# Kernel optimization log

Hardware: AMD Instinct MI355X
Metric: run time of the kernel (lower is better)

## Reference

```python
import jax, jax.numpy as jnp
import numpy as np

NUM_GROUPS = 32
EPS = 1e-5


def group_norm(x, w, b):
    # x: [B, C, H, W]
    B, C, H, W = x.shape
    xg = x.reshape(B, NUM_GROUPS, C // NUM_GROUPS, H, W)
    mean = jnp.mean(xg, axis=(2, 3, 4), keepdims=True)
    var = jnp.var(xg, axis=(2, 3, 4), keepdims=True)
    xg = (xg - mean) * jax.lax.rsqrt(var + EPS)
    xn = xg.reshape(B, C, H, W)
    return xn * w[None, :, None, None] + b[None, :, None, None]


def conv1x1(x, w, b):
    # x: [B, C, H, W], w: [O, C], b: [O]
    return jnp.einsum('bchw,oc->bohw', x, w) + b[None, :, None, None]


def setup_inputs() -> dict:
    key = jax.random.key(0)
    ks = jax.random.split(key, 10)
    C = 512
    x = jax.random.normal(ks[0], (4, C, 64, 64), dtype=jnp.float32)
    s = 1.0 / np.sqrt(C)
    return {
        'x': x,
        'gn_w': jnp.ones((C,), jnp.float32),
        'gn_b': jnp.zeros((C,), jnp.float32),
        'q_w': jax.random.normal(ks[1], (C, C), jnp.float32) * s,
        'q_b': jax.random.normal(ks[2], (C,), jnp.float32) * 0.01,
        'k_w': jax.random.normal(ks[3], (C, C), jnp.float32) * s,
        'k_b': jax.random.normal(ks[4], (C,), jnp.float32) * 0.01,
        'v_w': jax.random.normal(ks[5], (C, C), jnp.float32) * s,
        'v_b': jax.random.normal(ks[6], (C,), jnp.float32) * 0.01,
        'p_w': jax.random.normal(ks[7], (C, C), jnp.float32) * s,
        'p_b': jax.random.normal(ks[8], (C,), jnp.float32) * 0.01,
    }


def reference(x, gn_w, gn_b, q_w, q_b, k_w, k_b, v_w, v_b, p_w, p_b):
    h_ = group_norm(x, gn_w, gn_b)
    q = conv1x1(h_, q_w, q_b)
    k = conv1x1(h_, k_w, k_b)
    v = conv1x1(h_, v_w, v_b)
    b, c, h, w = q.shape
    n = h * w
    q = q.reshape(b, c, n).transpose(0, 2, 1)   # [b, n, c]
    k = k.reshape(b, c, n)                       # [b, c, n]
    scores = jnp.einsum('bic,bcj->bij', q, k) * (c ** -0.5)  # [b, n, n]
    attn = jax.nn.softmax(scores, axis=-1)
    v = v.reshape(b, c, n)                       # [b, c, n]
    # h_[b,c,i] = sum_j v[b,c,j] * attn[b,i,j]
    h_out = jnp.einsum('bcj,bij->bci', v, attn).reshape(b, c, h, w)
    return x + conv1x1(h_out, p_w, p_b)
```

## Files before the change

kernel.cpp:

```cpp
#include <hip/hip_runtime.h>
#include <hip/hip_bf16.h>
#include <stdint.h>

#define AS1 __attribute__((address_space(1)))
#define AS3 __attribute__((address_space(3)))

typedef unsigned short ushort_t;
typedef __attribute__((ext_vector_type(8))) short short8;
typedef __attribute__((ext_vector_type(4))) float floatx4;
typedef __attribute__((ext_vector_type(16))) float floatx16;
typedef __attribute__((ext_vector_type(2))) unsigned int uint2v;

__device__ __forceinline__ ushort_t f2b(float f) {
    union { float f; unsigned int i; } x; x.f = f;
    unsigned int r = x.i + 0x7fffu + ((x.i >> 16) & 1u);
    return (ushort_t)(r >> 16);
}
__device__ __forceinline__ float b2f(ushort_t u) {
    union { unsigned int i; float f; } x; x.i = ((unsigned int)u) << 16; return x.f;
}
__device__ __forceinline__ void gl2lds16(const void* g, void* l) {
    __builtin_amdgcn_global_load_lds(
        (const AS1 unsigned int*)g,
        (AS3 unsigned int*)l,
        16, 0, 0);
}
__device__ __forceinline__ void plswap(unsigned& a, unsigned& b) {
#if __has_builtin(__builtin_amdgcn_permlane32_swap)
    uint2v r = __builtin_amdgcn_permlane32_swap(a, b, false, false);
    a = r.x; b = r.y;
#else
    asm volatile("v_permlane32_swap_b32 %0, %1" : "+v"(a), "+v"(b));
#endif
}

static constexpr int CCH = 512;
static constexpr int NSP = 4096;
static constexpr int NG  = 32;

__global__ __launch_bounds__(256) void gn_stats(const float* __restrict__ x,
                                                float* __restrict__ mean,
                                                float* __restrict__ rstd) {
    const long base = (long)blockIdx.x * 65536;
    const int t = threadIdx.x;
    float s1 = 0.f, s2 = 0.f;
    for (int i = t * 8; i < 65536; i += 256 * 8) {
        float4 a = *(const float4*)(x + base + i);
        float4 b = *(const float4*)(x + base + i + 4);
        s1 += a.x + a.y + a.z + a.w + b.x + b.y + b.z + b.w;
        s2 += a.x * a.x + a.y * a.y + a.z * a.z + a.w * a.w
            + b.x * b.x + b.y * b.y + b.z * b.z + b.w * b.w;
    }
#pragma unroll
    for (int o = 32; o; o >>= 1) { s1 += __shfl_xor(s1, o, 64); s2 += __shfl_xor(s2, o, 64); }
    __shared__ float r1[4], r2[4];
    const int lane = t & 63, wave = t >> 6;
    if (!lane) { r1[wave] = s1; r2[wave] = s2; }
    __syncthreads();
    if (!t) {
        float S1 = r1[0] + r1[1] + r1[2] + r1[3];
        float S2 = r2[0] + r2[1] + r2[2] + r2[3];
        float mu = S1 * (1.f / 65536.f);
        float var = S2 * (1.f / 65536.f) - mu * mu;
        mean[blockIdx.x] = mu;
        rstd[blockIdx.x] = rsqrtf(var + 1e-5f);
    }
}

__global__ __launch_bounds__(256) void w_to_bf16(const float* __restrict__ q,
                                                 const float* __restrict__ k,
                                                 const float* __restrict__ v,
                                                 const float* __restrict__ p,
                                                 const float* __restrict__ qb,
                                                 ushort_t* __restrict__ out,
                                                 float* __restrict__ sqb) {
    const float scl = 0.044194173824159216f;
    const float* srcs[4] = { q, k, v, p };
    const float* s = srcs[blockIdx.y];
    const float m = (blockIdx.y == 0) ? scl : 1.f;
    const long i = ((long)blockIdx.x * 256 + threadIdx.x) * 4;
    float4 f = *(const float4*)(s + i);
    ushort_t o[4] __attribute__((aligned(8)));
    o[0] = f2b(f.x * m); o[1] = f2b(f.y * m); o[2] = f2b(f.z * m); o[3] = f2b(f.w * m);
    *(ushort4*)(out + (long)blockIdx.y * 262144 + i) = *(ushort4*)o;
    if (blockIdx.y == 0 && blockIdx.x == 0 && threadIdx.x < 128) {
        const int j = threadIdx.x * 4;
        float4 b = *(const float4*)(qb + j);
        sqb[j] = b.x * scl; sqb[j + 1] = b.y * scl; sqb[j + 2] = b.z * scl; sqb[j + 3] = b.w * scl;
    }
}

__global__ __launch_bounds__(256) void norm_transpose(const float* __restrict__ x,
                                                      const float* __restrict__ gw,
                                                      const float* __restrict__ gb,
                                                      const float* __restrict__ mean,
                                                      const float* __restrict__ rstd,
                                                      ushort_t* __restrict__ ht) {
    __shared__ ushort_t tile[64 * 65];
    const int b = blockIdx.z, c0 = blockIdx.y * 64, n0 = blockIdx.x * 64;
    const int t = threadIdx.x;
    const float* xb = x + ((long)b * CCH + c0) * NSP + n0;
#pragma unroll
    for (int p = 0; p < 2; ++p) {
        int li = p * 2048 + t * 8;
        int cl = li >> 6, nl = li & 63;
        int c = c0 + cl, g = c >> 4;
        float mu = mean[b * NG + g], rs = rstd[b * NG + g];
        float w  = gw[c] * rs;
        float bb = gb[c] - mu * w;
        float4 a = *(const float4*)(xb + (long)cl * NSP + nl);
        float4 d = *(const float4*)(xb + (long)cl * NSP + nl + 4);
        float f[8] = { a.x, a.y, a.z, a.w, d.x, d.y, d.z, d.w };
#pragma unroll
        for (int j = 0; j < 8; ++j) tile[cl * 65 + nl + j] = f2b(f[j] * w + bb);
    }
    __syncthreads();
#pragma unroll
    for (int p = 0; p < 2; ++p) {
        int li = p * 2048 + t * 8;
        int nl = li >> 6, cl = li & 63;
        ushort_t v[8] __attribute__((aligned(16)));
#pragma unroll
        for (int j = 0; j < 8; ++j) v[j] = tile[(cl + j) * 65 + nl];
        *(uint4*)(ht + ((long)b * NSP + n0 + nl) * CCH + c0 + cl) = *(uint4*)v;
    }
}

template <int BIAS, int OUTF32, int RES>
__global__ __launch_bounds__(256, 2) void gemm_tn(
    const ushort_t* __restrict__ A, int lda, long sA,
    const ushort_t* __restrict__ B, int ldb, long sB,
    void* __restrict__ Cp, int ldc, long sC,
    const float* __restrict__ bias,
    const float* __restrict__ resid, long sR,
    float scale, int K) {
    __shared__ short As[128 * 32];
    __shared__ short Bs[128 * 32];
    const int t = threadIdx.x;
    const int lane = t & 63, wave = t >> 6;
    const long bz = blockIdx.z;
    const int m0 = blockIdx.y * 128, n0 = blockIdx.x * 128;

    const ushort_t* Ab = A + bz * sA + (long)(m0 + (t >> 2)) * lda + (t & 3) * 8;
    const ushort_t* Bb = B + bz * sB + (long)(n0 + (t >> 2)) * ldb + (t & 3) * 8;
    short* la = As + t * 8;
    short* lb = Bs + t * 8;

    const int wm = (wave & 1) * 64, wn = (wave >> 1) * 64;
    const int lm = lane & 15, lk = (lane >> 4) * 8;
    const short* pa = As + (wm + lm) * 32 + lk;
    const short* pb = Bs + (wn + lm) * 32 + lk;

    floatx4 acc[4][4];
#pragma unroll
    for (int i = 0; i < 4; ++i)
#pragma unroll
        for (int j = 0; j < 4; ++j) acc[i][j] = (floatx4){0.f, 0.f, 0.f, 0.f};

    for (int k0 = 0; k0 < K; k0 += 32) {
        __syncthreads();
        gl2lds16(Ab, la);
        gl2lds16(Ab + 64 * (long)lda, la + 64 * 32);
        gl2lds16(Bb, lb);
        gl2lds16(Bb + 64 * (long)ldb, lb + 64 * 32);
        Ab += 32; Bb += 32;
        __builtin_amdgcn_s_waitcnt(0);
        __syncthreads();
        short8 af[4], bfr[4];
#pragma unroll
        for (int i = 0; i < 4; ++i) af[i]  = *(const short8*)(pa + i * 16 * 32);
#pragma unroll
        for (int i = 0; i < 4; ++i) bfr[i] = *(const short8*)(pb + i * 16 * 32);
#pragma unroll
        for (int mi = 0; mi < 4; ++mi)
#pragma unroll
            for (int ni = 0; ni < 4; ++ni)
                acc[mi][ni] = __builtin_amdgcn_mfma_f32_16x16x32_bf16(af[mi], bfr[ni], acc[mi][ni], 0, 0, 0);
    }

    const int row4 = (lane >> 4) * 4;
    const int ncol = lane & 15;
#pragma unroll
    for (int mi = 0; mi < 4; ++mi) {
#pragma unroll
        for (int ni = 0; ni < 4; ++ni) {
            const int n = n0 + wn + ni * 16 + ncol;
            float bn = (BIAS == 2) ? bias[n] : 0.f;
#pragma unroll
            for (int r = 0; r < 4; ++r) {
                const int m = m0 + wm + mi * 16 + row4 + r;
                float v = acc[mi][ni][r] * scale;
                if (BIAS == 1) v += bias[m];
                if (BIAS == 2) v += bn;
                if (RES) v += resid[bz * sR + (long)m * ldc + n];
                const long idx = bz * sC + (long)m * ldc + n;
                if (OUTF32) ((float*)Cp)[idx] = v;
                else        ((ushort_t*)Cp)[idx] = f2b(v);
            }
        }
    }
}

__global__ __launch_bounds__(256, 1) void flash_attn(const ushort_t* __restrict__ Qt,
                                                     const ushort_t* __restrict__ Kt,
                                                     const ushort_t* __restrict__ V,
                                                     ushort_t* __restrict__ pO0,
                                                     ushort_t* __restrict__ pO1,
                                                     float* __restrict__ ml) {
    __shared__ short Klds[2 * 16384];
    __shared__ short Vlds[2 * 16384];
    const int t = threadIdx.x;
    const int lane = t & 63, wave = t >> 6;
    const int l31 = lane & 31, hi = lane >> 5;
    const int blk = blockIdx.x;
    const int xcd = blk & 7;
    const int bb = xcd >> 1;
    const int split = xcd & 1;
    const int rows0 = (blk >> 3) * 128 + wave * 32;
    const int j_lo = split * 2048;

    const ushort_t* Qb = Qt + ((long)bb * NSP + rows0 + l31) * CCH + hi * 8;
    short8 qf[32];
#pragma unroll
    for (int s = 0; s < 32; ++s) qf[s] = *(const short8*)(Qb + s * 16);

    floatx16 acc[16];
#pragma unroll
    for (int i = 0; i < 16; ++i)
        acc[i] = (floatx16){0.f,0.f,0.f,0.f,0.f,0.f,0.f,0.f,0.f,0.f,0.f,0.f,0.f,0.f,0.f,0.f};
    float lsum = 0.f;

    const ushort_t* KtB = Kt + (long)bb * NSP * CCH;
    const ushort_t* Vb  = V + (long)bb * NSP * CCH;

#define STAGE_K(buf, J0)                                                          \
    {                                                                             \
        short* kb_ = Klds + (buf) * 16384;                                        \
        _Pragma("unroll")                                                         \
        for (int i_ = 0; i_ < 8; ++i_) {                                          \
            const int ch_ = i_ * 256 + t;                                         \
            const int jr_ = ch_ >> 6, m_ = ch_ & 63;                              \
            const int ms_ = m_ ^ (jr_ & 15);                                      \
            gl2lds16(KtB + (long)((J0) + jr_) * CCH + ms_ * 8, kb_ + ch_ * 8);    \
        }                                                                         \
    }
#define STAGE_V(buf, J0)                                                          \
    {                                                                             \
        short* vb_ = Vlds + (buf) * 16384;                                        \
        _Pragma("unroll")                                                         \
        for (int i_ = 0; i_ < 8; ++i_) {                                          \
            const int g_ = i_ * 256 + t;                                          \
            const int d_ = g_ >> 2, mv_ = g_ & 3;                                 \
            const int js_ = (mv_ ^ ((d_ >> 1) & 3)) * 8;                          \
            gl2lds16(Vb + (long)d_ * NSP + (J0) + js_, vb_ + g_ * 8);             \
        }                                                                         \
    }

#define SOFTMAX_PACK(sS, PA0, PA1)                                                \
    {                                                                             \
        float pv_[16];                                                            \
        _Pragma("unroll")                                                         \
        for (int r = 0; r < 16; ++r) { pv_[r] = __expf((sS)[r] - 12.f); lsum += pv_[r]; } \
        unsigned pk[8];                                                           \
        _Pragma("unroll")                                                         \
        for (int g = 0; g < 4; ++g) {                                             \
            asm("v_cvt_pk_bf16_f32 %0, %1, %2" : "=v"(pk[2 * g])     : "v"(pv_[4 * g]),     "v"(pv_[4 * g + 1])); \
            asm("v_cvt_pk_bf16_f32 %0, %1, %2" : "=v"(pk[2 * g + 1]) : "v"(pv_[4 * g + 2]), "v"(pv_[4 * g + 3])); \
        }                                                                         \
        plswap(pk[0], pk[2]);                                                     \
        plswap(pk[1], pk[3]);                                                     \
        plswap(pk[4], pk[6]);                                                     \
        plswap(pk[5], pk[7]);                                                     \
        union { unsigned u[4]; short8 s8; } uA_, uB_;                             \
        uA_.u[0] = pk[0]; uA_.u[1] = pk[1]; uA_.u[2] = pk[2]; uA_.u[3] = pk[3];   \
        uB_.u[0] = pk[4]; uB_.u[1] = pk[5]; uB_.u[2] = pk[6]; uB_.u[3] = pk[7];   \
        (PA0) = uA_.s8; (PA1) = uB_.s8;                                           \
    }

    STAGE_K(0, j_lo);
    STAGE_V(0, j_lo);
    STAGE_K(1, j_lo + 32);
    __builtin_amdgcn_s_waitcnt(0);
    __syncthreads();

    const int exr = (l31 & 15) ^ hi;
    const short* kroot = Klds + l31 * 512;
    const int cv = (l31 >> 1) & 3;
    const int voff0 = l31 * 32 + ((hi ^ cv) << 3);
    const int voff1 = l31 * 32 + (((2 + hi) ^ cv) << 3);

    floatx16 sS = (floatx16){0.f,0.f,0.f,0.f,0.f,0.f,0.f,0.f,0.f,0.f,0.f,0.f,0.f,0.f,0.f,0.f};
#pragma unroll
    for (int s2 = 0; s2 < 16; ++s2) {
        short8 k0 = *(const short8*)(kroot + (((4 * s2)     ^ exr) << 3));
        short8 k1 = *(const short8*)(kroot + (((4 * s2 + 2) ^ exr) << 3));
        sS = __builtin_amdgcn_mfma_f32_32x32x16_bf16(k0, qf[2 * s2],     sS, 0, 0, 0);
        sS = __builtin_amdgcn_mfma_f32_32x32x16_bf16(k1, qf[2 * s2 + 1], sS, 0, 0, 0);
    }
    __syncthreads();

    int j0 = j_lo;
    for (int tile = 0; tile < 63; ++tile) {
        const int cur = tile & 1, nxt = cur ^ 1;
        if (tile < 62) STAGE_K(cur, j0 + 64);
        STAGE_V(nxt, j0 + 32);

        short8 PA0, PA1;
        SOFTMAX_PACK(sS, PA0, PA1);

        const short* kp  = kroot + nxt * 16384;
        const short* vp0 = Vlds + cur * 16384 + voff0;
        const short* vp1 = Vlds + cur * 16384 + voff1;
        floatx16 nS = (floatx16){0.f,0.f,0.f,0.f,0.f,0.f,0.f,0.f,0.f,0.f,0.f,0.f,0.f,0.f,0.f,0.f};
#pragma unroll
        for (int i = 0; i < 16; ++i) {
            short8 k0 = *(const short8*)(kp + (((4 * i)     ^ exr) << 3));
            short8 v0 = *(const short8*)(vp0 + i * 1024);
            nS = __builtin_amdgcn_mfma_f32_32x32x16_bf16(k0, qf[2 * i], nS, 0, 0, 0);
            acc[i] = __builtin_amdgcn_mfma_f32_32x32x16_bf16(PA0, v0, acc[i], 0, 0, 0);
            short8 k1 = *(const short8*)(kp + (((4 * i + 2) ^ exr) << 3));
            short8 v1 = *(const short8*)(vp1 + i * 1024);
            nS = __builtin_amdgcn_mfma_f32_32x32x16_bf16(k1, qf[2 * i + 1], nS, 0, 0, 0);
            acc[i] = __builtin_amdgcn_mfma_f32_32x32x16_bf16(PA1, v1, acc[i], 0, 0, 0);
        }
        sS = nS;
        __builtin_amdgcn_s_waitcnt(0);
        __syncthreads();
        j0 += 32;
    }

    {
        short8 PA0, PA1;
        SOFTMAX_PACK(sS, PA0, PA1);
        const short* vp0 = Vlds + 16384 + voff0;
        const short* vp1 = Vlds + 16384 + voff1;
#pragma unroll
        for (int i = 0; i < 16; ++i) {
            short8 v0 = *(const short8*)(vp0 + i * 1024);
            acc[i] = __builtin_amdgcn_mfma_f32_32x32x16_bf16(PA0, v0, acc[i], 0, 0, 0);
            short8 v1 = *(const short8*)(vp1 + i * 1024);
            acc[i] = __builtin_amdgcn_mfma_f32_32x32x16_bf16(PA1, v1, acc[i], 0, 0, 0);
        }
    }
#undef STAGE_K
#undef STAGE_V
#undef SOFTMAX_PACK

    const float lt = lsum + __shfl_xor(lsum, 32, 64);
    ushort_t* pOut = (split ? pO1 : pO0) + ((long)bb * NSP + rows0) * CCH;
#pragma unroll
    for (int dt = 0; dt < 16; ++dt)
#pragma unroll
        for (int r = 0; r < 16; ++r) {
            const int rl = (r & 3) + 8 * (r >> 2) + 4 * hi;
            pOut[(long)rl * CCH + dt * 32 + l31] = f2b(acc[dt][r]);
        }
    if (hi == 0) {
        ml[(long)split * 4 * NSP + (long)bb * NSP + rows0 + l31] = lt;
    }
}

__global__ __launch_bounds__(256) void merge_splits(ushort_t* __restrict__ pO0,
                                                    const ushort_t* __restrict__ pO1,
                                                    const float* __restrict__ ml) {
    const long f = ((long)blockIdx.x * 256 + threadIdx.x) * 8;
    const long row = f >> 9;
    const float inv = 1.f / (ml[row] + ml[(long)4 * NSP + row]);
    uint4 u0 = *(const uint4*)(pO0 + f);
    uint4 u1 = *(const uint4*)(pO1 + f);
    const unsigned int* a = (const unsigned int*)&u0;
    const unsigned int* b = (const unsigned int*)&u1;
    ushort_t out[8] __attribute__((aligned(16)));
#pragma unroll
    for (int i = 0; i < 4; ++i) {
        float x0 = __uint_as_float(a[i] << 16), y0 = __uint_as_float(a[i] & 0xffff0000u);
        float x1 = __uint_as_float(b[i] << 16), y1 = __uint_as_float(b[i] & 0xffff0000u);
        out[2 * i]     = f2b((x0 + x1) * inv);
        out[2 * i + 1] = f2b((y0 + y1) * inv);
    }
    *(uint4*)(pO0 + f) = *(uint4*)out;
}

extern "C" void kernel_launch(void* const* d_in, const int* in_sizes, int n_in,
                              void* d_out, int out_size, void* d_ws, size_t ws_size,
                              hipStream_t stream) {
    const float* x   = (const float*)d_in[0];
    const float* gnw = (const float*)d_in[1];
    const float* gnb = (const float*)d_in[2];
    const float* qw  = (const float*)d_in[3];
    const float* qb  = (const float*)d_in[4];
    const float* kw  = (const float*)d_in[5];
    const float* kb  = (const float*)d_in[6];
    const float* vw  = (const float*)d_in[7];
    const float* vb  = (const float*)d_in[8];
    const float* pw  = (const float*)d_in[9];
    const float* pb  = (const float*)d_in[10];
    float* out = (float*)d_out;
    (void)in_sizes; (void)n_in; (void)out_size; (void)ws_size;

    const long E = (long)NSP * CCH;
    char* ws = (char*)d_ws;
    float*    mean = (float*)ws;
    float*    rstd = (float*)(ws + 512);
    ushort_t* wb   = (ushort_t*)(ws + 1024);
    float*    sqb  = (float*)(wb + 4 * 262144);
    float*    ml   = sqb + 512;
    ushort_t* ht   = (ushort_t*)(ml + 2 * 4 * NSP);
    ushort_t* Kt   = ht + 4 * E;
    ushort_t* V    = Kt + 4 * E;
    ushort_t* Qt   = V  + 4 * E;
    ushort_t* hOT  = Qt + 4 * E;
    ushort_t* qwb = wb, *kwb = wb + 262144, *vwb = wb + 2 * 262144, *pwb = wb + 3 * 262144;

    gn_stats<<<128, 256, 0, stream>>>(x, mean, rstd);
    w_to_bf16<<<dim3(256, 4), 256, 0, stream>>>(qw, kw, vw, pw, qb, wb, sqb);
    norm_transpose<<<dim3(64, 8, 4), 256, 0, stream>>>(x, gnw, gnb, mean, rstd, ht);
    gemm_tn<2, 0, 0><<<dim3(4, 32, 4), 256, 0, stream>>>(ht, 512, E, qwb, 512, 0, Qt, 512, E, sqb, nullptr, 0, 1.f, 512);
    gemm_tn<2, 0, 0><<<dim3(4, 32, 4), 256, 0, stream>>>(ht, 512, E, kwb, 512, 0, Kt, 512, E, kb, nullptr, 0, 1.f, 512);
    gemm_tn<1, 0, 0><<<dim3(32, 4, 4), 256, 0, stream>>>(vwb, 512, 0, ht, 512, E, V, 4096, E, vb, nullptr, 0, 1.f, 512);
    flash_attn<<<256, 256, 0, stream>>>(Qt, Kt, V, hOT, ht, ml);
    merge_splits<<<4096, 256, 0, stream>>>(hOT, ht, ml);
    gemm_tn<1, 1, 1><<<dim3(32, 4, 4), 256, 0, stream>>>(pwb, 512, 0, hOT, 512, E,
                                                         out, 4096, E, pb, x, E, 1.f, 512);
}
```

Before: 375.5 us.

## Triple-buffer K tiles, split QK accumulator chains, relax barrier waitcnt

Adds a third K buffer in LDS so K is prefetched two tiles ahead. The end-of-tile wait becomes vmcnt(8), so the in-flight K loads for the next-next tile are not drained at each barrier. The QK^T accumulation is split into two independent MFMA chains (even/odd) that are summed inside the softmax, which shortens the dependent MFMA chain. LDS usage grows by 32 KB per block, and address computation moves to precomputed byte offsets.

```diff
diff --git a/kernel.cpp b/kernel.cpp
--- a/kernel.cpp
+++ b/kernel.cpp
@@ -207,7 +207,7 @@
                                                      ushort_t* __restrict__ pO0,
                                                      ushort_t* __restrict__ pO1,
                                                      float* __restrict__ ml) {
-    __shared__ short Klds[2 * 16384];
+    __shared__ short Klds[3 * 16384];
     __shared__ short Vlds[2 * 16384];
     const int t = threadIdx.x;
     const int lane = t & 63, wave = t >> 6;
@@ -233,9 +233,9 @@
     const ushort_t* KtB = Kt + (long)bb * NSP * CCH;
     const ushort_t* Vb  = V + (long)bb * NSP * CCH;
 
-#define STAGE_K(buf, J0)                                                          \
+#define STAGE_K(slot, J0)                                                         \
     {                                                                             \
-        short* kb_ = Klds + (buf) * 16384;                                        \
+        short* kb_ = Klds + (slot) * 16384;                                       \
         _Pragma("unroll")                                                         \
         for (int i_ = 0; i_ < 8; ++i_) {                                          \
             const int ch_ = i_ * 256 + t;                                         \
@@ -256,11 +256,11 @@
         }                                                                         \
     }
 
-#define SOFTMAX_PACK(sS, PA0, PA1)                                                \
+#define SOFTMAX_PACK(sE, sO, PA0, PA1)                                            \
     {                                                                             \
         float pv_[16];                                                            \
         _Pragma("unroll")                                                         \
-        for (int r = 0; r < 16; ++r) { pv_[r] = __expf((sS)[r] - 12.f); lsum += pv_[r]; } \
+        for (int r = 0; r < 16; ++r) { pv_[r] = __expf((sE)[r] + (sO)[r] - 12.f); lsum += pv_[r]; } \
         unsigned pk[8];                                                           \
         _Pragma("unroll")                                                         \
         for (int g = 0; g < 4; ++g) {                                             \
@@ -280,65 +280,86 @@
     STAGE_K(0, j_lo);
     STAGE_V(0, j_lo);
     STAGE_K(1, j_lo + 32);
+    STAGE_K(2, j_lo + 64);
     __builtin_amdgcn_s_waitcnt(0);
     __syncthreads();
 
     const int exr = (l31 & 15) ^ hi;
-    const short* kroot = Klds + l31 * 512;
+    const int eh = (exr >> 2) & 3, el = exr & 3;
+    int kb0_[4], kb1_[4];
+#pragma unroll
+    for (int r = 0; r < 4; ++r) {
+        kb0_[r] = l31 * 1024 + ((r ^ eh) << 6) + (el << 4);
+        kb1_[r] = l31 * 1024 + ((r ^ eh) << 6) + ((el ^ 2) << 4);
+    }
     const int cv = (l31 >> 1) & 3;
-    const int voff0 = l31 * 32 + ((hi ^ cv) << 3);
-    const int voff1 = l31 * 32 + (((2 + hi) ^ cv) << 3);
-
-    floatx16 sS = (floatx16){0.f,0.f,0.f,0.f,0.f,0.f,0.f,0.f,0.f,0.f,0.f,0.f,0.f,0.f,0.f,0.f};
-#pragma unroll
-    for (int s2 = 0; s2 < 16; ++s2) {
-        short8 k0 = *(const short8*)(kroot + (((4 * s2)     ^ exr) << 3));
-        short8 k1 = *(const short8*)(kroot + (((4 * s2 + 2) ^ exr) << 3));
-        sS = __builtin_amdgcn_mfma_f32_32x32x16_bf16(k0, qf[2 * s2],     sS, 0, 0, 0);
-        sS = __builtin_amdgcn_mfma_f32_32x32x16_bf16(k1, qf[2 * s2 + 1], sS, 0, 0, 0);
+    const int vb0 = l31 * 64 + ((hi ^ cv) << 4);
+    const int vb1 = l31 * 64 + (((2 + hi) ^ cv) << 4);
+
+    floatx16 sSE = (floatx16){0.f,0.f,0.f,0.f,0.f,0.f,0.f,0.f,0.f,0.f,0.f,0.f,0.f,0.f,0.f,0.f};
+    floatx16 sSO = sSE;
+#pragma unroll
+    for (int i = 0; i < 16; ++i) {
+        short8 k0 = *(const short8*)((const char*)Klds + (kb0_[i & 3] + (i >> 2) * 256));
+        short8 k1 = *(const short8*)((const char*)Klds + (kb1_[i & 3] + (i >> 2) * 256));
+        sSE = __builtin_amdgcn_mfma_f32_32x32x16_bf16(k0, qf[2 * i],     sSE, 0, 0, 0);
+        sSO = __builtin_amdgcn_mfma_f32_32x32x16_bf16(k1, qf[2 * i + 1], sSO, 0, 0, 0);
     }
     __syncthreads();
 
     int j0 = j_lo;
+    int ksw = 0, ksr = 1;
     for (int tile = 0; tile < 63; ++tile) {
         const int cur = tile & 1, nxt = cur ^ 1;
-        if (tile < 62) STAGE_K(cur, j0 + 64);
         STAGE_V(nxt, j0 + 32);
+        if (tile <= 60) STAGE_K(ksw, j0 + 96);
 
         short8 PA0, PA1;
-        SOFTMAX_PACK(sS, PA0, PA1);
-
-        const short* kp  = kroot + nxt * 16384;
-        const short* vp0 = Vlds + cur * 16384 + voff0;
-        const short* vp1 = Vlds + cur * 16384 + voff1;
-        floatx16 nS = (floatx16){0.f,0.f,0.f,0.f,0.f,0.f,0.f,0.f,0.f,0.f,0.f,0.f,0.f,0.f,0.f,0.f};
+        SOFTMAX_PACK(sSE, sSO, PA0, PA1);
+
+        const int slotB = ksr * 32768, curB = cur * 32768;
+        int ka0_[4], ka1_[4];
+#pragma unroll
+        for (int r = 0; r < 4; ++r) { ka0_[r] = kb0_[r] + slotB; ka1_[r] = kb1_[r] + slotB; }
+        const int va0 = vb0 + curB, va1 = vb1 + curB;
+
+        floatx16 nE = (floatx16){0.f,0.f,0.f,0.f,0.f,0.f,0.f,0.f,0.f,0.f,0.f,0.f,0.f,0.f,0.f,0.f};
+        floatx16 nO = nE;
 #pragma unroll
         for (int i = 0; i < 16; ++i) {
-            short8 k0 = *(const short8*)(kp + (((4 * i)     ^ exr) << 3));
-            short8 v0 = *(const short8*)(vp0 + i * 1024);
-            nS = __builtin_amdgcn_mfma_f32_32x32x16_bf16(k0, qf[2 * i], nS, 0, 0, 0);
+            short8 k0 = *(const short8*)((const char*)Klds + (ka0_[i & 3] + (i >> 2) * 256));
+            short8 v0 = *(const short8*)((const char*)Vlds + (va0 + i * 2048));
+            nE = __builtin_amdgcn_mfma_f32_32x32x16_bf16(k0, qf[2 * i], nE, 0, 0, 0);
             acc[i] = __builtin_amdgcn_mfma_f32_32x32x16_bf16(PA0, v0, acc[i], 0, 0, 0);
-            short8 k1 = *(const short8*)(kp + (((4 * i + 2) ^ exr) << 3));
-            short8 v1 = *(const short8*)(vp1 + i * 1024);
-            nS = __builtin_amdgcn_mfma_f32_32x32x16_bf16(k1, qf[2 * i + 1], nS, 0, 0, 0);
+            short8 k1 = *(const short8*)((const char*)Klds + (ka1_[i & 3] + (i >> 2) * 256));
+            short8 v1 = *(const short8*)((const char*)Vlds + (va1 + i * 2048));
+            nO = __builtin_amdgcn_mfma_f32_32x32x16_bf16(k1, qf[2 * i + 1], nO, 0, 0, 0);
             acc[i] = __builtin_amdgcn_mfma_f32_32x32x16_bf16(PA1, v1, acc[i], 0, 0, 0);
         }
-        sS = nS;
-        __builtin_amdgcn_s_waitcnt(0);
-        __syncthreads();
+        sSE = nE; sSO = nO;
+
+        if (tile <= 60) {
+            asm volatile("s_waitcnt vmcnt(8)" ::: "memory");
+            __builtin_amdgcn_sched_barrier(0);
+            __builtin_amdgcn_s_barrier();
+        } else {
+            __builtin_amdgcn_s_waitcnt(0);
+            __syncthreads();
+        }
         j0 += 32;
+        ksw = (ksw == 2) ? 0 : ksw + 1;
+        ksr = (ksr == 2) ? 0 : ksr + 1;
     }
 
     {
         short8 PA0, PA1;
-        SOFTMAX_PACK(sS, PA0, PA1);
-        const short* vp0 = Vlds + 16384 + voff0;
-        const short* vp1 = Vlds + 16384 + voff1;
+        SOFTMAX_PACK(sSE, sSO, PA0, PA1);
+        const int va0 = vb0 + 32768, va1 = vb1 + 32768;
 #pragma unroll
         for (int i = 0; i < 16; ++i) {
-            short8 v0 = *(const short8*)(vp0 + i * 1024);
+            short8 v0 = *(const short8*)((const char*)Vlds + (va0 + i * 2048));
             acc[i] = __builtin_amdgcn_mfma_f32_32x32x16_bf16(PA0, v0, acc[i], 0, 0, 0);
-            short8 v1 = *(const short8*)(vp1 + i * 1024);
+            short8 v1 = *(const short8*)((const char*)Vlds + (va1 + i * 2048));
             acc[i] = __builtin_amdgcn_mfma_f32_32x32x16_bf16(PA1, v1, acc[i], 0, 0, 0);
         }
     }
```

New measurement: 446.9 us. 1.19x slower.
